# Performance work log

Hardware: AMD Instinct MI355X
Metric: run time of the kernel (lower is better)

## Reference

```python
import jax, jax.numpy as jnp
import numpy as np

N_NODES = 50000
N_EDGES = 800000
D = 64


def setup_inputs() -> dict:
    key = jax.random.key(0)
    k1, k2, k3, k4, k5 = jax.random.split(key, 5)
    feat = jax.random.normal(k1, (N_NODES, D), dtype=jnp.float32)
    h_e = jax.random.normal(k2, (1, D), dtype=jnp.float32)
    W = jax.random.normal(k3, (D, D), dtype=jnp.float32) * (1.0 / np.sqrt(D))
    src = jax.random.randint(k4, (N_EDGES,), 0, N_NODES, dtype=jnp.int32)
    dst = jax.random.randint(k5, (N_EDGES,), 0, N_NODES, dtype=jnp.int32)
    return {"feat": feat, "h_e": h_e, "W": W, "src": src, "dst": dst}


def reference(feat, h_e, W, src, dst):
    # CompConv with comp_fn='sub', norm='right', linear=True, no bias/activation.
    n_nodes = feat.shape[0]
    # edge gather + compose: comp_h[e] = feat[src[e]] - h_e  (E, D)
    comp_h = feat[src] - h_e
    # shared linear transform on edge messages (E, D_out)
    m = comp_h @ W
    # scatter-sum messages to destination nodes (N, D_out)
    rst = jax.ops.segment_sum(m, dst, num_segments=n_nodes)
    # 'right' norm: divide by in-degree (clamped to >= 1)
    degs = jax.ops.segment_sum(jnp.ones_like(dst, dtype=jnp.float32), dst,
                               num_segments=n_nodes)
    degs = jnp.maximum(degs, 1.0)
    return rst / degs[:, None]
```

## Files before the change

kernel.cpp:

```cpp
#include <hip/hip_runtime.h>

#define DIM 64
#define NPB 128
#define NPB_LOG 7
#define MAXNB 512

typedef unsigned short ushort_t;
typedef float f32x4 __attribute__((ext_vector_type(4)));


__device__ __forceinline__ ushort_t f2bf_rne(float f) {
    const unsigned u = __float_as_uint(f);
    return (ushort_t)((u + 0x7FFFu + ((u >> 16) & 1u)) >> 16);
}

__global__ void __launch_bounds__(256)
cc_convert(const float* __restrict__ feat, ushort_t* __restrict__ featb, int n_elems) {
    int i = (blockIdx.x * blockDim.x + threadIdx.x) * 4;
    const int stride = gridDim.x * blockDim.x * 4;
    for (; i + 3 < n_elems; i += stride) {
        const float4 v = *(const float4*)&feat[i];
        ushort4 o;
        o.x = f2bf_rne(v.x); o.y = f2bf_rne(v.y);
        o.z = f2bf_rne(v.z); o.w = f2bf_rne(v.w);
        *(ushort4*)&featb[i] = o;
    }
}

__global__ void __launch_bounds__(256)
cc_count(const int* __restrict__ dst, int* __restrict__ ccnt, int n_edges, int nb) {
    __shared__ int lc[MAXNB];
    for (int i = threadIdx.x; i < nb; i += 256) lc[i] = 0;
    __syncthreads();
    int i = blockIdx.x * blockDim.x + threadIdx.x;
    const int stride = gridDim.x * blockDim.x;
    for (; i < n_edges; i += stride)
        atomicAdd(&lc[dst[i] >> NPB_LOG], 1);
    __syncthreads();
    for (int i = threadIdx.x; i < nb; i += 256)
        if (lc[i]) atomicAdd(&ccnt[i], lc[i]);
}

__global__ void __launch_bounds__(256)
cc_scan(const int* __restrict__ ccnt, int* __restrict__ coff, int* __restrict__ ccur,
        int nb, int* __restrict__ offsets, int n_nodes) {
    __shared__ int wsum[4];
    const int tid = threadIdx.x, lane = tid & 63, wid = tid >> 6;
    const int i0 = tid * 2;
    const int v0 = (i0 < nb) ? ccnt[i0] : 0;
    const int v1 = (i0 + 1 < nb) ? ccnt[i0 + 1] : 0;
    const int t = v0 + v1;
    int incl = t;
    for (int off = 1; off < 64; off <<= 1) {
        const int u = __shfl_up(incl, off, 64);
        if (lane >= off) incl += u;
    }
    if (lane == 63) wsum[wid] = incl;
    __syncthreads();
    int wbase = 0;
    for (int w = 0; w < wid; ++w) wbase += wsum[w];
    const int ex = wbase + incl - t;
    if (i0 < nb)     { coff[i0]     = ex;      ccur[i0]     = ex; }
    if (i0 + 1 < nb) { coff[i0 + 1] = ex + v0; ccur[i0 + 1] = ex + v0; }
    if (tid == 255) {
        const int total = wbase + incl;
        coff[nb] = total;
        offsets[n_nodes] = total;
    }
}

__global__ void __launch_bounds__(256)
cc_scatter(const int* __restrict__ src, const int* __restrict__ dst,
           int* __restrict__ ccur, int* __restrict__ packed,
           int n_edges, int nb) {
    __shared__ int lc[MAXNB];
    __shared__ int lbase[MAXNB];
    const int ch = (n_edges + gridDim.x - 1) / gridDim.x;
    const int lo = blockIdx.x * ch;
    const int hi = min(lo + ch, n_edges);
    for (int i = threadIdx.x; i < nb; i += 256) lc[i] = 0;
    __syncthreads();
    for (int i = lo + threadIdx.x; i < hi; i += 256)
        atomicAdd(&lc[dst[i] >> NPB_LOG], 1);
    __syncthreads();
    for (int i = threadIdx.x; i < nb; i += 256) {
        const int c = lc[i];
        lbase[i] = c ? atomicAdd(&ccur[i], c) : 0;
        lc[i] = 0;
    }
    __syncthreads();
    for (int i = lo + threadIdx.x; i < hi; i += 256) {
        const int d = dst[i];
        const int b = d >> NPB_LOG;
        const int p = lbase[b] + atomicAdd(&lc[b], 1);
        packed[p] = (int)(((unsigned)d << 16) | (unsigned)src[i]);
    }
}

__global__ void __launch_bounds__(256)
cc_build(const int* __restrict__ coff, const int* __restrict__ packed,
         int* __restrict__ offsets, int* __restrict__ edge_src, int n_nodes) {
    __shared__ int deg[NPB];
    __shared__ int loff[NPB];
    __shared__ int wsum2[2];
    const int b = blockIdx.x;
    const int nlo = b << NPB_LOG;
    const int e0 = coff[b], e1 = coff[b + 1];
    const int tid = threadIdx.x, lane = tid & 63, wid = tid >> 6;

    if (tid < NPB) deg[tid] = 0;
    __syncthreads();
    for (int i = e0 + tid; i < e1; i += 256)
        atomicAdd(&deg[(((unsigned)packed[i]) >> 16) & (NPB - 1)], 1);
    __syncthreads();

    int v = 0, incl = 0;
    if (tid < NPB) {
        v = deg[tid];
        incl = v;
        for (int off = 1; off < 64; off <<= 1) {
            const int u = __shfl_up(incl, off, 64);
            if (lane >= off) incl += u;
        }
        if (lane == 63) wsum2[wid] = incl;
    }
    __syncthreads();
    if (tid < NPB) {
        const int ex = incl - v + ((wid == 1) ? wsum2[0] : 0);
        loff[tid] = ex;
        if (nlo + tid < n_nodes) offsets[nlo + tid] = e0 + ex;
        deg[tid] = 0;
    }
    __syncthreads();
    for (int i = e0 + tid; i < e1; i += 256) {
        const int pk = packed[i];
        const int l = (((unsigned)pk) >> 16) & (NPB - 1);
        const int pos = e0 + loff[l] + atomicAdd(&deg[l], 1);
        edge_src[pos] = pk & 0xFFFF;
    }
}

#define ADD8(a, q)                                          \
    {                                                       \
        a[0] += __uint_as_float((q).x << 16);               \
        a[1] += __uint_as_float((q).x & 0xFFFF0000u);       \
        a[2] += __uint_as_float((q).y << 16);               \
        a[3] += __uint_as_float((q).y & 0xFFFF0000u);       \
        a[4] += __uint_as_float((q).z << 16);               \
        a[5] += __uint_as_float((q).z & 0xFFFF0000u);       \
        a[6] += __uint_as_float((q).w << 16);               \
        a[7] += __uint_as_float((q).w & 0xFFFF0000u);       \
    }

__global__ void __launch_bounds__(256)
cc_gather8(const ushort_t* __restrict__ featb, const int* __restrict__ offsets,
           const int* __restrict__ edge_src, float* __restrict__ agg,
           int n_nodes) {
    const int lane = threadIdx.x & 63;
    const int g    = lane >> 3;
    const int dq   = lane & 7;

    const int wave   = (blockIdx.x * blockDim.x + threadIdx.x) >> 6;
    const int nwaves = (gridDim.x * blockDim.x) >> 6;
    for (int nb = wave * 8; nb < n_nodes; nb += nwaves * 8) {
        const int n = nb + g;
        const bool valid = (n < n_nodes);
        const int e0 = valid ? offsets[n] : 0;
        const int e1 = valid ? offsets[n + 1] : 0;
        float a[8] = {0.f, 0.f, 0.f, 0.f, 0.f, 0.f, 0.f, 0.f};
        int e = e0;
        for (; e + 2 <= e1; e += 2) {
            const int s0 = edge_src[e];
            const int s1 = edge_src[e + 1];
            const uint4 q0 = *(const uint4*)&featb[(size_t)s0 * DIM + dq * 8];
            const uint4 q1 = *(const uint4*)&featb[(size_t)s1 * DIM + dq * 8];
            ADD8(a, q0);
            ADD8(a, q1);
        }
        if (e < e1) {
            const int s = edge_src[e];
            const uint4 q = *(const uint4*)&featb[(size_t)s * DIM + dq * 8];
            ADD8(a, q);
        }
        if (valid) {
            f32x4 v0 = {a[0], a[1], a[2], a[3]};
            f32x4 v1 = {a[4], a[5], a[6], a[7]};
            *(f32x4*)&agg[(size_t)n * DIM + dq * 8]     = v0;
            *(f32x4*)&agg[(size_t)n * DIM + dq * 8 + 4] = v1;
        }
    }
}

__global__ void __launch_bounds__(256)
cc_xform(const float* __restrict__ Wg, const float* __restrict__ h_e,
         const int* __restrict__ offsets, float* __restrict__ io, int n_nodes) {
    __shared__ float Wl[DIM * DIM];
    __shared__ float At[64][68];
    __shared__ float heWl[DIM];

    const int t = threadIdx.x;
    for (int i = t * 4; i < DIM * DIM; i += 256 * 4)
        *(float4*)&Wl[i] = *(const float4*)&Wg[i];
    __syncthreads();

    if (t < DIM) {
        float s = 0.f;
        for (int k = 0; k < DIM; ++k) s += h_e[k] * Wl[k * DIM + t];
        heWl[t] = s;
    }

    const int n0 = blockIdx.x * 64;
    const int r = t >> 2;
    const int q = t & 3;
    if (n0 + r < n_nodes) {
        const float4* srcp = (const float4*)&io[(size_t)(n0 + r) * DIM + q * 16];
        const float4 v0 = srcp[0], v1 = srcp[1], v2 = srcp[2], v3 = srcp[3];
        *(float4*)&At[r][q * 16 + 0]  = v0;
        *(float4*)&At[r][q * 16 + 4]  = v1;
        *(float4*)&At[r][q * 16 + 8]  = v2;
        *(float4*)&At[r][q * 16 + 12] = v3;
    }
    __syncthreads();

    const int tx = t & 15, ty = t >> 4;
    float acc[4][4] = {{0.f}};
#pragma unroll 8
    for (int k = 0; k < DIM; ++k) {
        const float4 bv = *(const float4*)&Wl[k * DIM + tx * 4];
        const float a0 = At[ty * 4 + 0][k];
        const float a1 = At[ty * 4 + 1][k];
        const float a2 = At[ty * 4 + 2][k];
        const float a3 = At[ty * 4 + 3][k];
        acc[0][0] += a0 * bv.x; acc[0][1] += a0 * bv.y; acc[0][2] += a0 * bv.z; acc[0][3] += a0 * bv.w;
        acc[1][0] += a1 * bv.x; acc[1][1] += a1 * bv.y; acc[1][2] += a1 * bv.z; acc[1][3] += a1 * bv.w;
        acc[2][0] += a2 * bv.x; acc[2][1] += a2 * bv.y; acc[2][2] += a2 * bv.z; acc[2][3] += a2 * bv.w;
        acc[3][0] += a3 * bv.x; acc[3][1] += a3 * bv.y; acc[3][2] += a3 * bv.z; acc[3][3] += a3 * bv.w;
    }

    const float hw0 = heWl[tx * 4 + 0], hw1 = heWl[tx * 4 + 1];
    const float hw2 = heWl[tx * 4 + 2], hw3 = heWl[tx * 4 + 3];
#pragma unroll
    for (int i = 0; i < 4; ++i) {
        const int n = n0 + ty * 4 + i;
        if (n < n_nodes) {
            const float dg = (float)(offsets[n + 1] - offsets[n]);
            const float rd = 1.0f / fmaxf(dg, 1.0f);
            float4 o;
            o.x = (acc[i][0] - dg * hw0) * rd;
            o.y = (acc[i][1] - dg * hw1) * rd;
            o.z = (acc[i][2] - dg * hw2) * rd;
            o.w = (acc[i][3] - dg * hw3) * rd;
            *(float4*)&io[(size_t)n * DIM + tx * 4] = o;
        }
    }
}

__global__ void __launch_bounds__(256)
compconv_hist(const int* __restrict__ dst, int* __restrict__ deg_i, int n_edges) {
    int i = blockIdx.x * blockDim.x + threadIdx.x;
    const int stride = gridDim.x * blockDim.x;
    for (; i < n_edges; i += stride)
        atomicAdd(&deg_i[dst[i]], 1);
}

__global__ void __launch_bounds__(1024)
compconv_scan1(const int* __restrict__ deg_i, int* __restrict__ offsets,
               int* __restrict__ cursor, int n) {
    __shared__ int wsum[16];
    __shared__ int s_carry;
    const int tid = threadIdx.x, lane = tid & 63, wid = tid >> 6;
    if (tid == 0) s_carry = 0;
    __syncthreads();
    const int CHUNK = 1024 * 4;
    for (int base = 0; base < n; base += CHUNK) {
        const int idx = base + tid * 4;
        int4 v = make_int4(0, 0, 0, 0);
        if (idx + 3 < n) v = *(const int4*)&deg_i[idx];
        else {
            if (idx + 0 < n) v.x = deg_i[idx + 0];
            if (idx + 1 < n) v.y = deg_i[idx + 1];
            if (idx + 2 < n) v.z = deg_i[idx + 2];
            if (idx + 3 < n) v.w = deg_i[idx + 3];
        }
        const int t = v.x + v.y + v.z + v.w;
        int incl = t;
        for (int off = 1; off < 64; off <<= 1) {
            const int u = __shfl_up(incl, off, 64);
            if (lane >= off) incl += u;
        }
        if (lane == 63) wsum[wid] = incl;
        __syncthreads();
        if (wid == 0) {
            const int w = (lane < 16) ? wsum[lane] : 0;
            int winc = w;
            for (int off = 1; off < 16; off <<= 1) {
                const int u = __shfl_up(winc, off, 64);
                if (lane >= off) winc += u;
            }
            if (lane < 16) wsum[lane] = winc - w;
        }
        __syncthreads();
        const int ex = s_carry + wsum[wid] + (incl - t);
        if (idx + 3 < n) {
            const int4 ov = make_int4(ex, ex + v.x, ex + v.x + v.y, ex + v.x + v.y + v.z);
            *(int4*)&offsets[idx] = ov;
            *(int4*)&cursor[idx]  = ov;
        } else {
            if (idx + 0 < n) { offsets[idx+0] = ex;               cursor[idx+0] = offsets[idx+0]; }
            if (idx + 1 < n) { offsets[idx+1] = ex+v.x;           cursor[idx+1] = offsets[idx+1]; }
            if (idx + 2 < n) { offsets[idx+2] = ex+v.x+v.y;       cursor[idx+2] = offsets[idx+2]; }
            if (idx + 3 < n) { offsets[idx+3] = ex+v.x+v.y+v.z;   cursor[idx+3] = offsets[idx+3]; }
        }
        __syncthreads();
        if (tid == 1023) s_carry = ex + t;
        __syncthreads();
    }
    if (tid == 0) offsets[n] = s_carry;
}

__global__ void __launch_bounds__(256)
compconv_bucket(const int* __restrict__ src, const int* __restrict__ dst,
                int* __restrict__ cursor, int* __restrict__ edge_src, int n_edges) {
    int i = blockIdx.x * blockDim.x + threadIdx.x;
    const int stride = gridDim.x * blockDim.x;
    for (; i < n_edges; i += stride) {
        const int p = atomicAdd(&cursor[dst[i]], 1);
        edge_src[p] = src[i];
    }
}

__global__ void __launch_bounds__(256)
compconv_gather(const float* __restrict__ feat, const float* __restrict__ Wg,
                const float* __restrict__ h_e, const int* __restrict__ offsets,
                const int* __restrict__ edge_src, float* __restrict__ out,
                int n_nodes) {
    __shared__ float Wl[DIM * DIM];
    for (int i = threadIdx.x * 4; i < DIM * DIM; i += blockDim.x * 4)
        *(float4*)&Wl[i] = *(const float4*)&Wg[i];
    __syncthreads();

    const int lane = threadIdx.x & 63;
    const int g    = lane >> 4;
    const int dq   = lane & 15;

    const float he = h_e[lane];
    float heW = 0.0f;
#pragma unroll
    for (int k = 0; k < DIM; ++k)
        heW += __shfl(he, k, 64) * Wl[k * DIM + lane];

    const int wave   = (blockIdx.x * blockDim.x + threadIdx.x) >> 6;
    const int nwaves = (gridDim.x * blockDim.x) >> 6;
    for (int n = wave; n < n_nodes; n += nwaves) {
        const int e0 = offsets[n];
        const int e1 = offsets[n + 1];
        float ax = 0.0f, ay = 0.0f, az = 0.0f, aw = 0.0f;
        int e = e0;
        for (; e + 8 <= e1; e += 8) {
            const int s0 = edge_src[e + g];
            const int s1 = edge_src[e + 4 + g];
            const float4 a = *(const float4*)&feat[(size_t)s0 * DIM + dq * 4];
            const float4 b = *(const float4*)&feat[(size_t)s1 * DIM + dq * 4];
            ax += a.x + b.x; ay += a.y + b.y; az += a.z + b.z; aw += a.w + b.w;
        }
        if (e + 4 <= e1) {
            const int s = edge_src[e + g];
            const float4 a = *(const float4*)&feat[(size_t)s * DIM + dq * 4];
            ax += a.x; ay += a.y; az += a.z; aw += a.w;
            e += 4;
        }
        if (g < e1 - e) {
            const int s = edge_src[e + g];
            const float4 a = *(const float4*)&feat[(size_t)s * DIM + dq * 4];
            ax += a.x; ay += a.y; az += a.z; aw += a.w;
        }
        ax += __shfl_xor(ax, 16, 64); ay += __shfl_xor(ay, 16, 64);
        az += __shfl_xor(az, 16, 64); aw += __shfl_xor(aw, 16, 64);
        ax += __shfl_xor(ax, 32, 64); ay += __shfl_xor(ay, 32, 64);
        az += __shfl_xor(az, 32, 64); aw += __shfl_xor(aw, 32, 64);

        float s = 0.0f;
#pragma unroll
        for (int q = 0; q < 16; ++q) {
            const float a0 = __shfl(ax, q, 64);
            const float a1 = __shfl(ay, q, 64);
            const float a2 = __shfl(az, q, 64);
            const float a3 = __shfl(aw, q, 64);
            s += a0 * Wl[(4 * q + 0) * DIM + lane]
               + a1 * Wl[(4 * q + 1) * DIM + lane]
               + a2 * Wl[(4 * q + 2) * DIM + lane]
               + a3 * Wl[(4 * q + 3) * DIM + lane];
        }
        const float dg = (float)(e1 - e0);
        out[(size_t)n * DIM + lane] = (s - dg * heW) / fmaxf(dg, 1.0f);
    }
}

extern "C" void kernel_launch(void* const* d_in, const int* in_sizes, int n_in,
                              void* d_out, int out_size, void* d_ws, size_t ws_size,
                              hipStream_t stream) {
    const float* feat = (const float*)d_in[0];
    const float* h_e  = (const float*)d_in[1];
    const float* W    = (const float*)d_in[2];
    const int*   src  = (const int*)d_in[3];
    const int*   dst  = (const int*)d_in[4];

    const int n_edges = in_sizes[3];
    const int n_nodes = in_sizes[0] / DIM;

    float* out = (float*)d_out;

    const int nb = (n_nodes + NPB - 1) >> NPB_LOG;
    const int n_off_pad = (n_nodes + 4) & ~3;

    const size_t need_cc = ((size_t)(512 + 512 + 516) + n_off_pad + n_edges) * sizeof(int);
    const size_t need_bf = need_cc + (size_t)n_nodes * DIM * sizeof(ushort_t);
    const bool primary_ok = (n_nodes <= 65536) && (nb <= MAXNB) &&
                            (out_size >= n_nodes * DIM) && (out_size >= n_edges) &&
                            (ws_size >= need_bf);

    if (primary_ok) {
        int* ccnt     = (int*)d_ws;
        int* ccur     = ccnt + 512;
        int* coff     = ccur + 512;
        int* offsets  = coff + 516;
        int* edge_src = offsets + n_off_pad;
        ushort_t* featb = (ushort_t*)(edge_src + n_edges);
        int* packed   = (int*)d_out;
        float* agg    = out;

        cc_convert<<<1024, 256, 0, stream>>>(feat, featb, n_nodes * DIM);
        hipMemsetAsync(ccnt, 0, 512 * sizeof(int), stream);
        cc_count  <<<256, 256, 0, stream>>>(dst, ccnt, n_edges, nb);
        cc_scan   <<<1,   256, 0, stream>>>(ccnt, coff, ccur, nb, offsets, n_nodes);
        cc_scatter<<<256, 256, 0, stream>>>(src, dst, ccur, packed, n_edges, nb);
        cc_build  <<<nb,  256, 0, stream>>>(coff, packed, offsets, edge_src, n_nodes);

        const int gblocks = (n_nodes + 31) / 32;
        cc_gather8<<<gblocks, 256, 0, stream>>>(featb, offsets, edge_src, agg, n_nodes);
        const int xblocks = (n_nodes + 63) / 64;
        cc_xform  <<<xblocks, 256, 0, stream>>>(W, h_e, offsets, out, n_nodes);
    } else {
        int* deg_i    = (int*)d_ws;
        int* cursor   = deg_i + n_nodes;
        int* offsets  = cursor + n_nodes;
        int* edge_src = offsets + (n_nodes + 1);

        hipMemsetAsync(deg_i, 0, (size_t)n_nodes * sizeof(int), stream);
        compconv_hist<<<1024, 256, 0, stream>>>(dst, deg_i, n_edges);
        compconv_scan1<<<1, 1024, 0, stream>>>(deg_i, offsets, cursor, n_nodes);
        compconv_bucket<<<1024, 256, 0, stream>>>(src, dst, cursor, edge_src, n_edges);
        compconv_gather<<<2048, 256, 0, stream>>>(feat, W, h_e, offsets, edge_src,
                                                  out, n_nodes);
    }
}
```

Measured before the change: 83.76 us.

## Fuse per-bucket CSR build, gather and linear transform into one kernel

New measurement: 77.43 us, median of 2. 1.08x faster.

```diff
diff --git a/kernel.cpp b/kernel.cpp
--- a/kernel.cpp
+++ b/kernel.cpp
@@ -1,9 +1,10 @@
 #include <hip/hip_runtime.h>
 
 #define DIM 64
-#define NPB 128
-#define NPB_LOG 7
-#define MAXNB 512
+#define NPB 64
+#define NPB_LOG 6
+#define MAXNB 1024
+#define ECAP 2048
 
 typedef unsigned short ushort_t;
 typedef float f32x4 __attribute__((ext_vector_type(4)));
@@ -15,7 +16,10 @@
 }
 
 __global__ void __launch_bounds__(256)
-cc_convert(const float* __restrict__ feat, ushort_t* __restrict__ featb, int n_elems) {
+cc_prep(const float* __restrict__ feat, ushort_t* __restrict__ featb,
+        int n_elems, int* __restrict__ ccnt) {
+    if (blockIdx.x == 0)
+        for (int i = threadIdx.x; i < MAXNB; i += 256) ccnt[i] = 0;
     int i = (blockIdx.x * blockDim.x + threadIdx.x) * 4;
     const int stride = gridDim.x * blockDim.x * 4;
     for (; i + 3 < n_elems; i += stride) {
@@ -43,14 +47,16 @@
 
 __global__ void __launch_bounds__(256)
 cc_scan(const int* __restrict__ ccnt, int* __restrict__ coff, int* __restrict__ ccur,
-        int nb, int* __restrict__ offsets, int n_nodes) {
+        int nb) {
     __shared__ int wsum[4];
     const int tid = threadIdx.x, lane = tid & 63, wid = tid >> 6;
-    const int i0 = tid * 2;
-    const int v0 = (i0 < nb) ? ccnt[i0] : 0;
+    const int i0 = tid * 4;
+    const int v0 = (i0     < nb) ? ccnt[i0]     : 0;
     const int v1 = (i0 + 1 < nb) ? ccnt[i0 + 1] : 0;
-    const int t = v0 + v1;
-    int incl = t;
+    const int v2 = (i0 + 2 < nb) ? ccnt[i0 + 2] : 0;
+    const int v3 = (i0 + 3 < nb) ? ccnt[i0 + 3] : 0;
+    const int tt = v0 + v1 + v2 + v3;
+    int incl = tt;
     for (int off = 1; off < 64; off <<= 1) {
         const int u = __shfl_up(incl, off, 64);
         if (lane >= off) incl += u;
@@ -59,14 +65,12 @@
     __syncthreads();
     int wbase = 0;
     for (int w = 0; w < wid; ++w) wbase += wsum[w];
-    const int ex = wbase + incl - t;
-    if (i0 < nb)     { coff[i0]     = ex;      ccur[i0]     = ex; }
-    if (i0 + 1 < nb) { coff[i0 + 1] = ex + v0; ccur[i0 + 1] = ex + v0; }
-    if (tid == 255) {
-        const int total = wbase + incl;
-        coff[nb] = total;
-        offsets[n_nodes] = total;
-    }
+    const int ex = wbase + incl - tt;
+    if (i0     < nb) { coff[i0]     = ex;                ccur[i0]     = ex; }
+    if (i0 + 1 < nb) { coff[i0 + 1] = ex + v0;           ccur[i0 + 1] = ex + v0; }
+    if (i0 + 2 < nb) { coff[i0 + 2] = ex + v0 + v1;      ccur[i0 + 2] = ex + v0 + v1; }
+    if (i0 + 3 < nb) { coff[i0 + 3] = ex + v0 + v1 + v2; ccur[i0 + 3] = ex + v0 + v1 + v2; }
+    if (tid == 255) coff[nb] = wbase + incl;
 }
 
 __global__ void __launch_bounds__(256)
@@ -94,49 +98,6 @@
         const int b = d >> NPB_LOG;
         const int p = lbase[b] + atomicAdd(&lc[b], 1);
         packed[p] = (int)(((unsigned)d << 16) | (unsigned)src[i]);
-    }
-}
-
-__global__ void __launch_bounds__(256)
-cc_build(const int* __restrict__ coff, const int* __restrict__ packed,
-         int* __restrict__ offsets, int* __restrict__ edge_src, int n_nodes) {
-    __shared__ int deg[NPB];
-    __shared__ int loff[NPB];
-    __shared__ int wsum2[2];
-    const int b = blockIdx.x;
-    const int nlo = b << NPB_LOG;
-    const int e0 = coff[b], e1 = coff[b + 1];
-    const int tid = threadIdx.x, lane = tid & 63, wid = tid >> 6;
-
-    if (tid < NPB) deg[tid] = 0;
-    __syncthreads();
-    for (int i = e0 + tid; i < e1; i += 256)
-        atomicAdd(&deg[(((unsigned)packed[i]) >> 16) & (NPB - 1)], 1);
-    __syncthreads();
-
-    int v = 0, incl = 0;
-    if (tid < NPB) {
-        v = deg[tid];
-        incl = v;
-        for (int off = 1; off < 64; off <<= 1) {
-            const int u = __shfl_up(incl, off, 64);
-            if (lane >= off) incl += u;
-        }
-        if (lane == 63) wsum2[wid] = incl;
-    }
-    __syncthreads();
-    if (tid < NPB) {
-        const int ex = incl - v + ((wid == 1) ? wsum2[0] : 0);
-        loff[tid] = ex;
-        if (nlo + tid < n_nodes) offsets[nlo + tid] = e0 + ex;
-        deg[tid] = 0;
-    }
-    __syncthreads();
-    for (int i = e0 + tid; i < e1; i += 256) {
-        const int pk = packed[i];
-        const int l = (((unsigned)pk) >> 16) & (NPB - 1);
-        const int pos = e0 + loff[l] + atomicAdd(&deg[l], 1);
-        edge_src[pos] = pk & 0xFFFF;
     }
 }
 
@@ -153,72 +114,99 @@
     }
 
 __global__ void __launch_bounds__(256)
-cc_gather8(const ushort_t* __restrict__ featb, const int* __restrict__ offsets,
-           const int* __restrict__ edge_src, float* __restrict__ agg,
-           int n_nodes) {
-    const int lane = threadIdx.x & 63;
-    const int g    = lane >> 3;
-    const int dq   = lane & 7;
-
-    const int wave   = (blockIdx.x * blockDim.x + threadIdx.x) >> 6;
-    const int nwaves = (gridDim.x * blockDim.x) >> 6;
-    for (int nb = wave * 8; nb < n_nodes; nb += nwaves * 8) {
-        const int n = nb + g;
-        const bool valid = (n < n_nodes);
-        const int e0 = valid ? offsets[n] : 0;
-        const int e1 = valid ? offsets[n + 1] : 0;
+cc_fused(const ushort_t* __restrict__ featb, const float* __restrict__ Wg,
+         const float* __restrict__ h_e, const int* __restrict__ coff,
+         const int* __restrict__ packed, float* __restrict__ out, int n_nodes) {
+    __shared__ float Wl[DIM * DIM];
+    __shared__ float At[NPB][DIM + 4];
+    __shared__ int   esl_in[ECAP];
+    __shared__ int   esl[ECAP];
+    __shared__ int   deg[NPB];
+    __shared__ int   loff[NPB];
+    __shared__ int   cur[NPB];
+    __shared__ float heWl[DIM];
+
+    const int t   = threadIdx.x;
+    const int b   = blockIdx.x;
+    const int e0  = coff[b];
+    const int cnt = coff[b + 1] - e0;
+    const bool fits = (cnt <= ECAP);
+
+    for (int i = t * 4; i < DIM * DIM; i += 1024)
+        *(float4*)&Wl[i] = *(const float4*)&Wg[i];
+    if (t < NPB) deg[t] = 0;
+    __syncthreads();
+
+    for (int i = t; i < cnt; i += 256) {
+        const int pk = packed[e0 + i];
+        if (fits) esl_in[i] = pk;
+        atomicAdd(&deg[(((unsigned)pk) >> 16) & (NPB - 1)], 1);
+    }
+    __syncthreads();
+
+    if (t < 64) {
+        const int v = deg[t];
+        int incl = v;
+        for (int off = 1; off < 64; off <<= 1) {
+            const int u = __shfl_up(incl, off, 64);
+            if (t >= off) incl += u;
+        }
+        loff[t] = incl - v;
+        cur[t]  = 0;
+    } else if (t < 128) {
+        const int c = t - 64;
+        float s = 0.f;
+        for (int k = 0; k < DIM; ++k) s += h_e[k] * Wl[k * DIM + c];
+        heWl[c] = s;
+    }
+    __syncthreads();
+
+    if (fits) {
+        for (int i = t; i < cnt; i += 256) {
+            const int pk = esl_in[i];
+            const int l  = (((unsigned)pk) >> 16) & (NPB - 1);
+            esl[loff[l] + atomicAdd(&cur[l], 1)] = pk & 0xFFFF;
+        }
+    }
+    __syncthreads();
+
+    const int grp = t >> 3;
+    const int dq  = t & 7;
+#pragma unroll
+    for (int half = 0; half < 2; ++half) {
+        const int l  = grp + half * 32;
+        const int d0 = loff[l];
+        const int dn = deg[l];
         float a[8] = {0.f, 0.f, 0.f, 0.f, 0.f, 0.f, 0.f, 0.f};
-        int e = e0;
-        for (; e + 2 <= e1; e += 2) {
-            const int s0 = edge_src[e];
-            const int s1 = edge_src[e + 1];
-            const uint4 q0 = *(const uint4*)&featb[(size_t)s0 * DIM + dq * 8];
-            const uint4 q1 = *(const uint4*)&featb[(size_t)s1 * DIM + dq * 8];
-            ADD8(a, q0);
-            ADD8(a, q1);
-        }
-        if (e < e1) {
-            const int s = edge_src[e];
-            const uint4 q = *(const uint4*)&featb[(size_t)s * DIM + dq * 8];
-            ADD8(a, q);
-        }
-        if (valid) {
-            f32x4 v0 = {a[0], a[1], a[2], a[3]};
-            f32x4 v1 = {a[4], a[5], a[6], a[7]};
-            *(f32x4*)&agg[(size_t)n * DIM + dq * 8]     = v0;
-            *(f32x4*)&agg[(size_t)n * DIM + dq * 8 + 4] = v1;
-        }
-    }
-}
-
-__global__ void __launch_bounds__(256)
-cc_xform(const float* __restrict__ Wg, const float* __restrict__ h_e,
-         const int* __restrict__ offsets, float* __restrict__ io, int n_nodes) {
-    __shared__ float Wl[DIM * DIM];
-    __shared__ float At[64][68];
-    __shared__ float heWl[DIM];
-
-    const int t = threadIdx.x;
-    for (int i = t * 4; i < DIM * DIM; i += 256 * 4)
-        *(float4*)&Wl[i] = *(const float4*)&Wg[i];
-    __syncthreads();
-
-    if (t < DIM) {
-        float s = 0.f;
-        for (int k = 0; k < DIM; ++k) s += h_e[k] * Wl[k * DIM + t];
-        heWl[t] = s;
-    }
-
-    const int n0 = blockIdx.x * 64;
-    const int r = t >> 2;
-    const int q = t & 3;
-    if (n0 + r < n_nodes) {
-        const float4* srcp = (const float4*)&io[(size_t)(n0 + r) * DIM + q * 16];
-        const float4 v0 = srcp[0], v1 = srcp[1], v2 = srcp[2], v3 = srcp[3];
-        *(float4*)&At[r][q * 16 + 0]  = v0;
-        *(float4*)&At[r][q * 16 + 4]  = v1;
-        *(float4*)&At[r][q * 16 + 8]  = v2;
-        *(float4*)&At[r][q * 16 + 12] = v3;
+        if (fits) {
+            int e = 0;
+            for (; e + 2 <= dn; e += 2) {
+                const int s0 = esl[d0 + e];
+                const int s1 = esl[d0 + e + 1];
+                const uint4 q0 = *(const uint4*)&featb[(size_t)s0 * DIM + dq * 8];
+                const uint4 q1 = *(const uint4*)&featb[(size_t)s1 * DIM + dq * 8];
+                ADD8(a, q0);
+                ADD8(a, q1);
+            }
+            if (e < dn) {
+                const int s = esl[d0 + e];
+                const uint4 q = *(const uint4*)&featb[(size_t)s * DIM + dq * 8];
+                ADD8(a, q);
+            }
+        } else {
+            for (int i = 0; i < cnt; ++i) {
+                const int pk = packed[e0 + i];
+                if ((int)((((unsigned)pk) >> 16) & (NPB - 1)) == l) {
+                    const uint4 q =
+                        *(const uint4*)&featb[(size_t)(pk & 0xFFFF) * DIM + dq * 8];
+                    ADD8(a, q);
+                }
+            }
+        }
+        const f32x4 v0 = {a[0], a[1], a[2], a[3]};
+        const f32x4 v1 = {a[4], a[5], a[6], a[7]};
+        *(f32x4*)&At[l][dq * 8]     = v0;
+        *(f32x4*)&At[l][dq * 8 + 4] = v1;
     }
     __syncthreads();
 
@@ -236,21 +224,21 @@
         acc[2][0] += a2 * bv.x; acc[2][1] += a2 * bv.y; acc[2][2] += a2 * bv.z; acc[2][3] += a2 * bv.w;
         acc[3][0] += a3 * bv.x; acc[3][1] += a3 * bv.y; acc[3][2] += a3 * bv.z; acc[3][3] += a3 * bv.w;
     }
-
     const float hw0 = heWl[tx * 4 + 0], hw1 = heWl[tx * 4 + 1];
     const float hw2 = heWl[tx * 4 + 2], hw3 = heWl[tx * 4 + 3];
+    const int n0 = b << NPB_LOG;
 #pragma unroll
     for (int i = 0; i < 4; ++i) {
         const int n = n0 + ty * 4 + i;
         if (n < n_nodes) {
-            const float dg = (float)(offsets[n + 1] - offsets[n]);
+            const float dg = (float)deg[ty * 4 + i];
             const float rd = 1.0f / fmaxf(dg, 1.0f);
             float4 o;
             o.x = (acc[i][0] - dg * hw0) * rd;
             o.y = (acc[i][1] - dg * hw1) * rd;
             o.z = (acc[i][2] - dg * hw2) * rd;
             o.w = (acc[i][3] - dg * hw3) * rd;
-            *(float4*)&io[(size_t)n * DIM + tx * 4] = o;
+            *(float4*)&out[(size_t)n * DIM + tx * 4] = o;
         }
     }
 }
@@ -410,36 +398,25 @@
 
     float* out = (float*)d_out;
 
-    const int nb = (n_nodes + NPB - 1) >> NPB_LOG;
-    const int n_off_pad = (n_nodes + 4) & ~3;
-
-    const size_t need_cc = ((size_t)(512 + 512 + 516) + n_off_pad + n_edges) * sizeof(int);
-    const size_t need_bf = need_cc + (size_t)n_nodes * DIM * sizeof(ushort_t);
-    const bool primary_ok = (n_nodes <= 65536) && (nb <= MAXNB) &&
-                            (out_size >= n_nodes * DIM) && (out_size >= n_edges) &&
-                            (ws_size >= need_bf);
+    const int nb   = (n_nodes + NPB - 1) >> NPB_LOG;
+    const int epad = (n_edges + 3) & ~3;
+
+    const size_t need = ((size_t)(1024 + 1024 + 1028) + epad) * sizeof(int) +
+                        (size_t)n_nodes * DIM * sizeof(ushort_t);
+    const bool primary_ok = (n_nodes <= 65536) && (nb <= MAXNB) && (ws_size >= need);
 
     if (primary_ok) {
-        int* ccnt     = (int*)d_ws;
-        int* ccur     = ccnt + 512;
-        int* coff     = ccur + 512;
-        int* offsets  = coff + 516;
-        int* edge_src = offsets + n_off_pad;
-        ushort_t* featb = (ushort_t*)(edge_src + n_edges);
-        int* packed   = (int*)d_out;
-        float* agg    = out;
-
-        cc_convert<<<1024, 256, 0, stream>>>(feat, featb, n_nodes * DIM);
-        hipMemsetAsync(ccnt, 0, 512 * sizeof(int), stream);
-        cc_count  <<<256, 256, 0, stream>>>(dst, ccnt, n_edges, nb);
-        cc_scan   <<<1,   256, 0, stream>>>(ccnt, coff, ccur, nb, offsets, n_nodes);
-        cc_scatter<<<256, 256, 0, stream>>>(src, dst, ccur, packed, n_edges, nb);
-        cc_build  <<<nb,  256, 0, stream>>>(coff, packed, offsets, edge_src, n_nodes);
-
-        const int gblocks = (n_nodes + 31) / 32;
-        cc_gather8<<<gblocks, 256, 0, stream>>>(featb, offsets, edge_src, agg, n_nodes);
-        const int xblocks = (n_nodes + 63) / 64;
-        cc_xform  <<<xblocks, 256, 0, stream>>>(W, h_e, offsets, out, n_nodes);
+        int* ccnt   = (int*)d_ws;
+        int* ccur   = ccnt + 1024;
+        int* coff   = ccur + 1024;
+        int* packed = coff + 1028;
+        ushort_t* featb = (ushort_t*)(packed + epad);
+
+        cc_prep   <<<1024, 256, 0, stream>>>(feat, featb, n_nodes * DIM, ccnt);
+        cc_count  <<<256,  256, 0, stream>>>(dst, ccnt, n_edges, nb);
+        cc_scan   <<<1,    256, 0, stream>>>(ccnt, coff, ccur, nb);
+        cc_scatter<<<256,  256, 0, stream>>>(src, dst, ccur, packed, n_edges, nb);
+        cc_fused  <<<nb,   256, 0, stream>>>(featb, W, h_e, coff, packed, out, n_nodes);
     } else {
         int* deg_i    = (int*)d_ws;
         int* cursor   = deg_i + n_nodes;
```
